# Kernel tuning notes

Measured on AMD Instinct MI355X. Metric: run time of the kernel, lower is better.

The kernel has to match this reference:

```python
import jax, jax.numpy as jnp
import numpy as np

B, L, D, MAXL = 4, 2048, 1024, 4096

def setup_inputs() -> dict:
    key = jax.random.key(0)
    ks = jax.random.split(key, 7)
    x = jax.random.normal(ks[0], (B, L, D), dtype=jnp.float32)
    mask = jnp.ones((B, 1, L), dtype=jnp.int32)
    # kv_proj: Linear(D,D) -> ReLU -> Linear(D, 2D)
    s1 = 1.0 / np.sqrt(D)
    W1 = jax.random.uniform(ks[1], (D, D), minval=-s1, maxval=s1, dtype=jnp.float32)
    b1 = jax.random.uniform(ks[2], (D,), minval=-s1, maxval=s1, dtype=jnp.float32)
    W2 = jax.random.uniform(ks[3], (D, 2 * D), minval=-s1, maxval=s1, dtype=jnp.float32)
    b2 = jax.random.uniform(ks[4], (2 * D,), minval=-s1, maxval=s1, dtype=jnp.float32)
    D_to_L = jax.random.normal(ks[5], (D, MAXL), dtype=jnp.float32) * 0.01
    return {"x": x, "mask": mask, "W1": W1, "b1": b1, "W2": W2, "b2": b2, "D_to_L": D_to_L}

def reference(x, mask, W1, b1, W2, b2, D_to_L):
    Lcur = x.shape[1]
    h = jax.nn.relu(x @ W1 + b1)          # [B,L,D]
    kv = h @ W2 + b2                       # [B,L,2D]
    k, value = jnp.split(kv, 2, axis=-1)   # [B,L,D] each
    scores = jnp.einsum('bld,dk->blk', k, D_to_L[:, :Lcur])  # [B,L,L]
    scores = jnp.where(mask == 0, -jnp.inf, scores)
    attention = jax.nn.softmax(scores, axis=-1)
    output = attention @ value             # [B,L,D]
    return output, attention
```

## Files before the change

kernel.cpp:

```cpp
#include <hip/hip_runtime.h>
#include <cstdint>
#include <cstddef>

__device__ __forceinline__ float bf2f(uint16_t u) {
    union { uint32_t i; float f; } w; w.i = ((uint32_t)u) << 16; return w.f;
}
__device__ __forceinline__ uint16_t f2bf(float f) {
    union { float f; uint32_t i; } w; w.f = f;
    uint32_t x = w.i;
    uint32_t r = (x + 0x7FFFu + ((x >> 16) & 1u)) >> 16;
    return (uint16_t)r;
}

typedef __bf16 bf16x8 __attribute__((ext_vector_type(8)));
typedef float  f32x4  __attribute__((ext_vector_type(4)));

__device__ __forceinline__ void load_lds16(const void* gptr, void* lptr) {
    __builtin_amdgcn_global_load_lds(
        (__attribute__((address_space(1))) void*)gptr,
        (__attribute__((address_space(3))) void*)lptr,
        16, 0, 0);
}

template<int AFP32, int OUTFP32, int RELU>
__global__ __launch_bounds__(256, 3)
void gemm_bt(const void* __restrict__ Av, const uint16_t* __restrict__ BT,
             const float* __restrict__ bias, void* __restrict__ Cv,
             int K, int lda, int ldb, int ldc,
             long long sA, long long sB, long long sC)
{
    __shared__ uint16_t As[128 * 32];
    __shared__ uint16_t Bs[128 * 32];

    const int nx = (int)gridDim.x, ny = (int)gridDim.y, nz = (int)gridDim.z;
    const int g   = (int)blockIdx.x + nx * ((int)blockIdx.y + ny * (int)blockIdx.z);
    const int xcd = g & 7;
    const int ii  = g >> 3;
    const int xz  = 8 / nz;
    const int bz  = xcd / xz;
    const int sub = xcd % xz;
    const int ypc = ny / xz;
    const int by  = sub * ypc + ii % ypc;
    const int bx  = ii / ypc;

    const int t    = threadIdx.x;
    const int lane = t & 63;
    const int w    = t >> 6;
    const int quad = lane >> 4;
    const int l15  = lane & 15;
    const int wr   = w >> 1;
    const int wc   = w & 1;
    const int gm0  = by * 128;
    const int gn0  = bx * 128;

    BT += (long long)bz * sB;

    f32x4 acc[4][4] = {};

    const int ch_r = lane >> 2;
    const int ch_c = (lane & 3) * 8;

    for (int k0 = 0; k0 < K; k0 += 32) {
        __syncthreads();

        {
            int row = w * 16 + ch_r;
            load_lds16(BT + (size_t)(gn0 + row) * ldb + k0 + ch_c, (void*)(Bs + w * 512));
            load_lds16(BT + (size_t)(gn0 + row + 64) * ldb + k0 + ch_c, (void*)(Bs + (w + 4) * 512));
        }
        if (AFP32) {
            const float* A = (const float*)Av + (long long)bz * sA;
            const int row = t >> 1, half = t & 1;
            const float* ap = A + (size_t)(gm0 + row) * lda + k0 + half * 16;
            float4 f0 = ((const float4*)ap)[0];
            float4 f1 = ((const float4*)ap)[1];
            float4 f2 = ((const float4*)ap)[2];
            float4 f3 = ((const float4*)ap)[3];
            union { __bf16 h[16]; uint4 q[2]; } u;
            u.h[0]  = (__bf16)f0.x; u.h[1]  = (__bf16)f0.y;
            u.h[2]  = (__bf16)f0.z; u.h[3]  = (__bf16)f0.w;
            u.h[4]  = (__bf16)f1.x; u.h[5]  = (__bf16)f1.y;
            u.h[6]  = (__bf16)f1.z; u.h[7]  = (__bf16)f1.w;
            u.h[8]  = (__bf16)f2.x; u.h[9]  = (__bf16)f2.y;
            u.h[10] = (__bf16)f2.z; u.h[11] = (__bf16)f2.w;
            u.h[12] = (__bf16)f3.x; u.h[13] = (__bf16)f3.y;
            u.h[14] = (__bf16)f3.z; u.h[15] = (__bf16)f3.w;
            uint4* d = (uint4*)(As + row * 32 + half * 16);
            d[0] = u.q[0];
            d[1] = u.q[1];
        } else {
            const uint16_t* A = (const uint16_t*)Av + (long long)bz * sA;
            int row = w * 16 + ch_r;
            load_lds16(A + (size_t)(gm0 + row) * lda + k0 + ch_c, (void*)(As + w * 512));
            load_lds16(A + (size_t)(gm0 + row + 64) * lda + k0 + ch_c, (void*)(As + (w + 4) * 512));
        }
        __syncthreads();

        bf16x8 af[4], bfr[4];
#pragma unroll
        for (int i = 0; i < 4; i++) {
            af[i]  = *(const bf16x8*)(As + (wr * 64 + i * 16 + l15) * 32 + quad * 8);
            bfr[i] = *(const bf16x8*)(Bs + (wc * 64 + i * 16 + l15) * 32 + quad * 8);
        }
#pragma unroll
        for (int mi = 0; mi < 4; mi++)
#pragma unroll
            for (int ni = 0; ni < 4; ni++)
                acc[mi][ni] = __builtin_amdgcn_mfma_f32_16x16x32_bf16(af[mi], bfr[ni], acc[mi][ni], 0, 0, 0);
    }

#pragma unroll
    for (int ni = 0; ni < 4; ni++) {
        const int gcol = gn0 + wc * 64 + ni * 16 + l15;
        const float bv = bias ? bias[gcol] : 0.0f;
#pragma unroll
        for (int mi = 0; mi < 4; mi++) {
#pragma unroll
            for (int r = 0; r < 4; r++) {
                const int grow = gm0 + wr * 64 + mi * 16 + quad * 4 + r;
                float v = acc[mi][ni][r] + bv;
                if (RELU) v = fmaxf(v, 0.0f);
                if (OUTFP32) {
                    float* C = (float*)Cv + (long long)bz * sC;
                    C[(size_t)grow * ldc + gcol] = v;
                } else {
                    uint16_t* C = (uint16_t*)Cv + (long long)bz * sC;
                    C[(size_t)grow * ldc + gcol] = f2bf(v);
                }
            }
        }
    }
}

__global__ __launch_bounds__(256)
void transpose_f32_to_bf16(const float* __restrict__ src, uint16_t* __restrict__ dst,
                           int src_ld, int dst_ld)
{
    __shared__ uint16_t tile[64 * 65];
    const int k0 = blockIdx.y * 64, n0 = blockIdx.x * 64;
    const int t = threadIdx.x;
#pragma unroll
    for (int i = 0; i < 16; i++) {
        int idx = i * 256 + t;
        int r = idx >> 6, c = idx & 63;
        tile[c * 65 + r] = f2bf(src[(size_t)(k0 + r) * src_ld + n0 + c]);
    }
    __syncthreads();
#pragma unroll
    for (int i = 0; i < 16; i++) {
        int idx = i * 256 + t;
        int n = idx >> 6, k = idx & 63;
        dst[(size_t)(n0 + n) * dst_ld + k0 + k] = tile[n * 65 + k];
    }
}

__global__ __launch_bounds__(256)
void transpose_bf16(const uint16_t* __restrict__ src, uint16_t* __restrict__ dst,
                    int src_ld, int dst_ld, long long sS, long long sD)
{
    __shared__ uint16_t tile[64 * 65];
    src += (long long)blockIdx.z * sS;
    dst += (long long)blockIdx.z * sD;
    const int k0 = blockIdx.y * 64, n0 = blockIdx.x * 64;
    const int t = threadIdx.x;
#pragma unroll
    for (int i = 0; i < 16; i++) {
        int idx = i * 256 + t;
        int r = idx >> 6, c = idx & 63;
        tile[c * 65 + r] = src[(size_t)(k0 + r) * src_ld + n0 + c];
    }
    __syncthreads();
#pragma unroll
    for (int i = 0; i < 16; i++) {
        int idx = i * 256 + t;
        int n = idx >> 6, k = idx & 63;
        dst[(size_t)(n0 + n) * dst_ld + k0 + k] = tile[n * 65 + k];
    }
}

__global__ __launch_bounds__(256)
void softmax_rows_f32(float* __restrict__ S, uint16_t* __restrict__ Sbf,
                      const int* __restrict__ mask, int L)
{
    const int row = blockIdx.x;
    const int b = row >> 11;
    float* rp = S + (size_t)row * L;
    uint16_t* bp = Sbf + (size_t)row * L;
    const int* mrow = mask + (size_t)b * L;
    const int t = threadIdx.x;
    const int c0 = t * 8;

    float v[8];
    *(float4*)(v + 0) = *(const float4*)(rp + c0);
    *(float4*)(v + 4) = *(const float4*)(rp + c0 + 4);
    bool mk[8];
    float lmax = -1e30f;
#pragma unroll
    for (int j = 0; j < 8; j++) {
        mk[j] = (mrow[c0 + j] != 0);
        if (mk[j]) lmax = fmaxf(lmax, v[j]);
    }
#pragma unroll
    for (int off = 32; off > 0; off >>= 1)
        lmax = fmaxf(lmax, __shfl_xor(lmax, off, 64));

    __shared__ float redm[4];
    __shared__ float reds[4];
    const int w = t >> 6, lane = t & 63;
    if (lane == 0) redm[w] = lmax;
    __syncthreads();
    lmax = fmaxf(fmaxf(redm[0], redm[1]), fmaxf(redm[2], redm[3]));

    float e[8];
    float lsum = 0.f;
#pragma unroll
    for (int j = 0; j < 8; j++) {
        e[j] = mk[j] ? __expf(v[j] - lmax) : 0.0f;
        lsum += e[j];
    }
#pragma unroll
    for (int off = 32; off > 0; off >>= 1)
        lsum += __shfl_xor(lsum, off, 64);
    if (lane == 0) reds[w] = lsum;
    __syncthreads();
    lsum = reds[0] + reds[1] + reds[2] + reds[3];

    const float inv = 1.0f / lsum;
    uint16_t ub[8];
#pragma unroll
    for (int j = 0; j < 8; j++) {
        v[j] = e[j] * inv;
        ub[j] = f2bf(v[j]);
    }
    *(float4*)(rp + c0)     = *(const float4*)(v + 0);
    *(float4*)(rp + c0 + 4) = *(const float4*)(v + 4);
    *(uint4*)(bp + c0)      = *(const uint4*)ub;
}

extern "C" void kernel_launch(void* const* d_in, const int* in_sizes, int n_in,
                              void* d_out, int out_size, void* d_ws, size_t ws_size,
                              hipStream_t stream)
{
    const float* x    = (const float*)d_in[0];
    const int*   mask = (const int*)d_in[1];
    const float* W1   = (const float*)d_in[2];
    const float* b1   = (const float*)d_in[3];
    const float* W2   = (const float*)d_in[4];
    const float* b2   = (const float*)d_in[5];
    const float* D2L  = (const float*)d_in[6];

    const int Lr = 2048, D = 1024, M = 4 * Lr;
    float* outp = (float*)d_out;
    float* attn = outp + (size_t)M * D;

    uint16_t* W1T  = (uint16_t*)d_ws;
    uint16_t* W2T  = W1T + 1024 * 1024;
    uint16_t* D2LT = W2T + 2048 * 1024;
    uint16_t* hbuf = D2LT + 2048 * 1024;
    uint16_t* kv   = hbuf + (size_t)M * D;
    uint16_t* vT   = hbuf;
    uint16_t* abf  = kv;

    dim3 blk(256);

    transpose_f32_to_bf16<<<dim3(16, 16), blk, 0, stream>>>(W1,  W1T,  1024, 1024);
    transpose_f32_to_bf16<<<dim3(32, 16), blk, 0, stream>>>(W2,  W2T,  2048, 1024);
    transpose_f32_to_bf16<<<dim3(32, 16), blk, 0, stream>>>(D2L, D2LT, 4096, 1024);

    gemm_bt<1, 0, 1><<<dim3(8, 64, 1), blk, 0, stream>>>(x, W1T, b1, hbuf,
        1024, 1024, 1024, 1024, 0, 0, 0);

    gemm_bt<0, 0, 0><<<dim3(16, 64, 1), blk, 0, stream>>>(hbuf, W2T, b2, kv,
        1024, 1024, 1024, 2048, 0, 0, 0);

    transpose_bf16<<<dim3(16, 32, 4), blk, 0, stream>>>(kv + 1024, vT,
        2048, 2048, (long long)2048 * 2048, (long long)1024 * 2048);

    gemm_bt<0, 1, 0><<<dim3(16, 64, 1), blk, 0, stream>>>(kv, D2LT, nullptr, attn,
        1024, 2048, 1024, 2048, 0, 0, 0);

    softmax_rows_f32<<<dim3(8192), blk, 0, stream>>>(attn, abf, mask, Lr);

    gemm_bt<0, 1, 0><<<dim3(8, 16, 4), blk, 0, stream>>>(abf, vT, nullptr, outp,
        2048, 2048, 2048, 1024,
        (long long)2048 * 2048, (long long)1024 * 2048, (long long)2048 * 1024);
}
```

Measured before the change: 356.4 us.

## Add 256x256 double-buffered GEMM kernel for kv and score projections

```diff
diff --git a/kernel.cpp b/kernel.cpp
--- a/kernel.cpp
+++ b/kernel.cpp
@@ -62,7 +62,6 @@
 
     for (int k0 = 0; k0 < K; k0 += 32) {
         __syncthreads();
-
         {
             int row = w * 16 + ch_r;
             load_lds16(BT + (size_t)(gn0 + row) * ldb + k0 + ch_c, (void*)(Bs + w * 512));
@@ -132,6 +131,122 @@
     }
 }
 
+template<int OUTFP32, int RELU>
+__global__ __launch_bounds__(512, 2)
+void gemm256_bt(const uint16_t* __restrict__ A, const uint16_t* __restrict__ BT,
+                const float* __restrict__ bias, void* __restrict__ Cv,
+                int K, int lda, int ldb, int ldc)
+{
+    extern __shared__ uint16_t lds[];
+
+    const int g   = (int)blockIdx.x + 8 * (int)blockIdx.y;
+    const int xcd = g & 7, ii = g >> 3;
+    const int by  = xcd * 4 + (ii & 3);
+    const int bx  = ii >> 2;
+    const int gm0 = by * 256, gn0 = bx * 256;
+
+    const int t    = threadIdx.x;
+    const int w    = t >> 6, lane = t & 63;
+    const int l15  = lane & 15, quad = lane >> 4;
+    const int wr   = w >> 2, wc = w & 3;
+
+    const int cpr  = quad ^ ((l15 >> 1) & 3);
+    const int arow = wr * 128 + l15;
+    const int brow = wc * 64 + l15;
+
+    const int r0 = t >> 2;
+    const int qg = (t & 3) ^ ((t >> 3) & 3);
+    const uint16_t* aS0 = A  + (size_t)(gm0 + r0) * lda + qg * 8;
+    const uint16_t* aS1 = aS0 + (size_t)128 * lda;
+    const uint16_t* bS0 = BT + (size_t)(gn0 + r0) * ldb + qg * 8;
+    const uint16_t* bS1 = bS0 + (size_t)128 * ldb;
+    const int ldst0 = (w * 64) * 8;
+    const int ldst1 = (512 + w * 64) * 8;
+
+#define SUBA(nb, kh) (lds + ((nb) * 2 + (kh)) * 8192)
+#define SUBB(nb, kh) (lds + 32768 + ((nb) * 2 + (kh)) * 8192)
+#define STAGE_A(nb, kh, k0s) do {                                              \
+        load_lds16(aS0 + (k0s) + (kh) * 32, (void*)(SUBA(nb, kh) + ldst0));    \
+        load_lds16(aS1 + (k0s) + (kh) * 32, (void*)(SUBA(nb, kh) + ldst1));    \
+    } while (0)
+#define STAGE_B(nb, kh, k0s) do {                                              \
+        load_lds16(bS0 + (k0s) + (kh) * 32, (void*)(SUBB(nb, kh) + ldst0));    \
+        load_lds16(bS1 + (k0s) + (kh) * 32, (void*)(SUBB(nb, kh) + ldst1));    \
+    } while (0)
+#define VMWAIT4 asm volatile("s_waitcnt vmcnt(4)" ::: "memory")
+#define NOWAIT  ((void)0)
+
+    f32x4 acc[8][4] = {};
+    bf16x8 bF[4];
+
+    STAGE_A(0, 0, 0); STAGE_B(0, 0, 0); STAGE_A(0, 1, 0); STAGE_B(0, 1, 0);
+    VMWAIT4;
+    __builtin_amdgcn_s_barrier();
+
+    const int NT = K >> 6;
+    for (int kt = 0; kt < NT; ++kt) {
+        const int buf = kt & 1, nb = buf ^ 1;
+        const int nk0 = (kt + 1 < NT) ? ((kt + 1) << 6) : 0;
+
+#define PHASE(kh, mh, STAGE_STMT, VM_STMT)                                          \
+        {                                                                           \
+            const uint16_t* As_ = SUBA(buf, kh);                                    \
+            const uint16_t* Bs_ = SUBB(buf, kh);                                    \
+            bf16x8 aF[4];                                                           \
+            _Pragma("unroll")                                                       \
+            for (int i = 0; i < 4; i++)                                             \
+                aF[i] = *(const bf16x8*)(As_ + (arow + (mh) * 64 + i * 16) * 32 + cpr * 8); \
+            if ((mh) == 0) {                                                        \
+                _Pragma("unroll")                                                   \
+                for (int ni = 0; ni < 4; ni++)                                      \
+                    bF[ni] = *(const bf16x8*)(Bs_ + (brow + ni * 16) * 32 + cpr * 8); \
+            }                                                                       \
+            STAGE_STMT;                                                             \
+            __builtin_amdgcn_s_barrier();                                           \
+            __builtin_amdgcn_s_setprio(1);                                          \
+            _Pragma("unroll")                                                       \
+            for (int i = 0; i < 4; i++)                                             \
+                _Pragma("unroll")                                                   \
+                for (int ni = 0; ni < 4; ni++)                                      \
+                    acc[(mh) * 4 + i][ni] = __builtin_amdgcn_mfma_f32_16x16x32_bf16( \
+                        aF[i], bF[ni], acc[(mh) * 4 + i][ni], 0, 0, 0);             \
+            __builtin_amdgcn_s_setprio(0);                                          \
+            VM_STMT;                                                                \
+            __builtin_amdgcn_s_barrier();                                           \
+        }
+
+        PHASE(0, 0, STAGE_A(nb, 0, nk0), NOWAIT)
+        PHASE(0, 1, STAGE_B(nb, 0, nk0), VMWAIT4)
+        PHASE(1, 0, STAGE_A(nb, 1, nk0), NOWAIT)
+        PHASE(1, 1, STAGE_B(nb, 1, nk0), VMWAIT4)
+#undef PHASE
+    }
+    asm volatile("s_waitcnt vmcnt(0)" ::: "memory");
+
+#pragma unroll
+    for (int ni = 0; ni < 4; ni++) {
+        const int gcol = gn0 + wc * 64 + ni * 16 + l15;
+        const float bv = bias ? bias[gcol] : 0.0f;
+#pragma unroll
+        for (int mi = 0; mi < 8; mi++) {
+#pragma unroll
+            for (int r = 0; r < 4; r++) {
+                const int grow = gm0 + wr * 128 + mi * 16 + quad * 4 + r;
+                float v = acc[mi][ni][r] + bv;
+                if (RELU) v = fmaxf(v, 0.0f);
+                if (OUTFP32) ((float*)Cv)[(size_t)grow * ldc + gcol] = v;
+                else         ((uint16_t*)Cv)[(size_t)grow * ldc + gcol] = f2bf(v);
+            }
+        }
+    }
+#undef SUBA
+#undef SUBB
+#undef STAGE_A
+#undef STAGE_B
+#undef VMWAIT4
+#undef NOWAIT
+}
+
 __global__ __launch_bounds__(256)
 void transpose_f32_to_bf16(const float* __restrict__ src, uint16_t* __restrict__ dst,
                            int src_ld, int dst_ld)
@@ -263,6 +378,11 @@
 
     dim3 blk(256);
 
+    hipFuncSetAttribute(reinterpret_cast<const void*>(&gemm256_bt<0, 0>),
+                        hipFuncAttributeMaxDynamicSharedMemorySize, 131072);
+    hipFuncSetAttribute(reinterpret_cast<const void*>(&gemm256_bt<1, 0>),
+                        hipFuncAttributeMaxDynamicSharedMemorySize, 131072);
+
     transpose_f32_to_bf16<<<dim3(16, 16), blk, 0, stream>>>(W1,  W1T,  1024, 1024);
     transpose_f32_to_bf16<<<dim3(32, 16), blk, 0, stream>>>(W2,  W2T,  2048, 1024);
     transpose_f32_to_bf16<<<dim3(32, 16), blk, 0, stream>>>(D2L, D2LT, 4096, 1024);
@@ -270,14 +390,14 @@
     gemm_bt<1, 0, 1><<<dim3(8, 64, 1), blk, 0, stream>>>(x, W1T, b1, hbuf,
         1024, 1024, 1024, 1024, 0, 0, 0);
 
-    gemm_bt<0, 0, 0><<<dim3(16, 64, 1), blk, 0, stream>>>(hbuf, W2T, b2, kv,
-        1024, 1024, 1024, 2048, 0, 0, 0);
+    gemm256_bt<0, 0><<<dim3(8, 32), dim3(512), 131072, stream>>>(hbuf, W2T, b2, kv,
+        1024, 1024, 1024, 2048);
 
     transpose_bf16<<<dim3(16, 32, 4), blk, 0, stream>>>(kv + 1024, vT,
         2048, 2048, (long long)2048 * 2048, (long long)1024 * 2048);
 
-    gemm_bt<0, 1, 0><<<dim3(16, 64, 1), blk, 0, stream>>>(kv, D2LT, nullptr, attn,
-        1024, 2048, 1024, 2048, 0, 0, 0);
+    gemm256_bt<1, 0><<<dim3(8, 32), dim3(512), 131072, stream>>>(kv, D2LT, nullptr, attn,
+        1024, 2048, 1024, 2048);
 
     softmax_rows_f32<<<dim3(8192), blk, 0, stream>>>(attn, abf, mask, Lr);
 
```

New measurement: 350.2 us. About the same (-1.8%).

## Replace GEMMs with 256-row double-buffered swizzled-LDS pipelined kernel

Applied to the files above, without the earlier changes.

```diff
diff --git a/kernel.cpp b/kernel.cpp
--- a/kernel.cpp
+++ b/kernel.cpp
@@ -2,9 +2,6 @@
 #include <cstdint>
 #include <cstddef>
 
-__device__ __forceinline__ float bf2f(uint16_t u) {
-    union { uint32_t i; float f; } w; w.i = ((uint32_t)u) << 16; return w.f;
-}
 __device__ __forceinline__ uint16_t f2bf(float f) {
     union { float f; uint32_t i; } w; w.f = f;
     uint32_t x = w.i;
@@ -22,114 +19,179 @@
         16, 0, 0);
 }
 
-template<int AFP32, int OUTFP32, int RELU>
-__global__ __launch_bounds__(256, 3)
-void gemm_bt(const void* __restrict__ Av, const uint16_t* __restrict__ BT,
+template<int BN, int OUTFP32, int RELU>
+__global__ __launch_bounds__(512, 2)
+void gemm256(const uint16_t* __restrict__ A, const uint16_t* __restrict__ BT,
              const float* __restrict__ bias, void* __restrict__ Cv,
              int K, int lda, int ldb, int ldc,
-             long long sA, long long sB, long long sC)
-{
-    __shared__ uint16_t As[128 * 32];
-    __shared__ uint16_t Bs[128 * 32];
-
-    const int nx = (int)gridDim.x, ny = (int)gridDim.y, nz = (int)gridDim.z;
-    const int g   = (int)blockIdx.x + nx * ((int)blockIdx.y + ny * (int)blockIdx.z);
-    const int xcd = g & 7;
-    const int ii  = g >> 3;
-    const int xz  = 8 / nz;
-    const int bz  = xcd / xz;
-    const int sub = xcd % xz;
-    const int ypc = ny / xz;
-    const int by  = sub * ypc + ii % ypc;
-    const int bx  = ii / ypc;
+             long long sB, int byShift)
+{
+    extern __shared__ uint16_t lds[];
+    constexpr int SB  = (BN == 256) ? 2 : 1;
+    constexpr int WN  = BN / 64;
+    constexpr int MI  = 2 * WN;
+    constexpr int SBE = BN * 32;
+
+    const int g   = (int)blockIdx.x + (int)gridDim.x * (int)blockIdx.y;
+    const int xcd = g & 7, ii = g >> 3;
+    const int by  = xcd * 4 + (ii & 3);
+    const int bx  = ii >> 2;
+    const int gm0 = by * 256, gn0 = bx * BN;
+    const int bz  = by >> byShift;
+    BT += (long long)bz * sB;
 
     const int t    = threadIdx.x;
-    const int lane = t & 63;
-    const int w    = t >> 6;
-    const int quad = lane >> 4;
-    const int l15  = lane & 15;
-    const int wr   = w >> 1;
-    const int wc   = w & 1;
-    const int gm0  = by * 128;
-    const int gn0  = bx * 128;
-
-    BT += (long long)bz * sB;
-
-    f32x4 acc[4][4] = {};
-
-    const int ch_r = lane >> 2;
-    const int ch_c = (lane & 3) * 8;
-
-    for (int k0 = 0; k0 < K; k0 += 32) {
-        __syncthreads();
-
-        {
-            int row = w * 16 + ch_r;
-            load_lds16(BT + (size_t)(gn0 + row) * ldb + k0 + ch_c, (void*)(Bs + w * 512));
-            load_lds16(BT + (size_t)(gn0 + row + 64) * ldb + k0 + ch_c, (void*)(Bs + (w + 4) * 512));
+    const int w    = t >> 6, lane = t & 63;
+    const int l15  = lane & 15, quad = lane >> 4;
+    const int wr   = w / WN, wc = w % WN;
+
+    const int cpr  = quad ^ ((l15 >> 1) & 3);
+    const int arow = wr * (32 * WN) + l15;
+    const int brow = wc * 64 + l15;
+
+    const int r0 = t >> 2;
+    const int qg = (t & 3) ^ ((t >> 3) & 3);
+    const uint16_t* aS0 = A  + (size_t)(gm0 + r0) * lda + qg * 8;
+    const uint16_t* aS1 = aS0 + (size_t)128 * lda;
+    const uint16_t* bS0 = BT + (size_t)(gn0 + r0) * ldb + qg * 8;
+    const uint16_t* bS1 = bS0 + (size_t)128 * ldb;
+    const int ldw = w * 512;
+
+#define SUBA(nb, kh) (lds + ((nb) * 2 + (kh)) * 8192)
+#define SUBB(nb, kh) (lds + 32768 + ((nb) * 2 + (kh)) * SBE)
+#define STAGE_A(nb, kh, k0s) do {                                               \
+        load_lds16(aS0 + (k0s) + (kh) * 32, (void*)(SUBA(nb, kh) + ldw));       \
+        load_lds16(aS1 + (k0s) + (kh) * 32, (void*)(SUBA(nb, kh) + 4096 + ldw));\
+    } while (0)
+#define STAGE_B(nb, kh, k0s) do {                                               \
+        load_lds16(bS0 + (k0s) + (kh) * 32, (void*)(SUBB(nb, kh) + ldw));       \
+        if constexpr (BN == 256)                                                \
+            load_lds16(bS1 + (k0s) + (kh) * 32,                                 \
+                       (void*)(SUBB(nb, kh) + 4096 + ldw));                     \
+    } while (0)
+#define VMW do {                                                                \
+        if constexpr (SB == 2) asm volatile("s_waitcnt vmcnt(4)" ::: "memory"); \
+        else                   asm volatile("s_waitcnt vmcnt(3)" ::: "memory"); \
+    } while (0)
+#define LGKM0 asm volatile("s_waitcnt lgkmcnt(0)" ::: "memory")
+#define NOWAIT ((void)0)
+
+    f32x4 acc[MI][4] = {};
+    bf16x8 bF[4];
+
+    STAGE_A(0, 0, 0); STAGE_B(0, 0, 0); STAGE_A(0, 1, 0); STAGE_B(0, 1, 0);
+    VMW;
+    __builtin_amdgcn_s_barrier();
+
+    const int NT = K >> 6;
+    for (int kt = 0; kt < NT; ++kt) {
+        const int buf = kt & 1, nb = buf ^ 1;
+        const int nk0 = (kt + 1 < NT) ? ((kt + 1) << 6) : 0;
+
+        if constexpr (BN == 256) {
+#define PHASE256(kh, mh, STAGE_STMT, VM_STMT)                                       \
+            {                                                                       \
+                const uint16_t* As_ = SUBA(buf, kh);                                \
+                const uint16_t* Bs_ = SUBB(buf, kh);                                \
+                bf16x8 aF[4];                                                       \
+                _Pragma("unroll")                                                   \
+                for (int i = 0; i < 4; i++)                                         \
+                    aF[i] = *(const bf16x8*)(As_ + (arow + (mh) * 64 + i * 16) * 32 + cpr * 8); \
+                if ((mh) == 0) {                                                    \
+                    _Pragma("unroll")                                               \
+                    for (int ni = 0; ni < 4; ni++)                                  \
+                        bF[ni] = *(const bf16x8*)(Bs_ + (brow + ni * 16) * 32 + cpr * 8); \
+                }                                                                   \
+                STAGE_STMT;                                                         \
+                __builtin_amdgcn_s_barrier();                                       \
+                LGKM0;                                                              \
+                __builtin_amdgcn_s_setprio(1);                                      \
+                _Pragma("unroll")                                                   \
+                for (int i = 0; i < 4; i++)                                         \
+                    _Pragma("unroll")                                               \
+                    for (int ni = 0; ni < 4; ni++)                                  \
+                        acc[(mh) * 4 + i][ni] = __builtin_amdgcn_mfma_f32_16x16x32_bf16( \
+                            aF[i], bF[ni], acc[(mh) * 4 + i][ni], 0, 0, 0);         \
+                __builtin_amdgcn_s_setprio(0);                                      \
+                VM_STMT;                                                            \
+                __builtin_amdgcn_s_barrier();                                       \
+            }
+            PHASE256(0, 0, STAGE_A(nb, 0, nk0), NOWAIT)
+            PHASE256(0, 1, STAGE_B(nb, 0, nk0), VMW)
+            PHASE256(1, 0, STAGE_A(nb, 1, nk0), NOWAIT)
+            PHASE256(1, 1, STAGE_B(nb, 1, nk0), VMW)
+#undef PHASE256
+        } else {
+#define PHASE128(kh)                                                                \
+            {                                                                       \
+                const uint16_t* As_ = SUBA(buf, kh);                                \
+                const uint16_t* Bs_ = SUBB(buf, kh);                                \
+                bf16x8 aF[4], bG[4];                                                \
+                _Pragma("unroll")                                                   \
+                for (int i = 0; i < 4; i++)                                         \
+                    aF[i] = *(const bf16x8*)(As_ + (arow + i * 16) * 32 + cpr * 8); \
+                _Pragma("unroll")                                                   \
+                for (int ni = 0; ni < 4; ni++)                                      \
+                    bG[ni] = *(const bf16x8*)(Bs_ + (brow + ni * 16) * 32 + cpr * 8); \
+                STAGE_A(nb, kh, nk0);                                               \
+                STAGE_B(nb, kh, nk0);                                               \
+                __builtin_amdgcn_s_barrier();                                       \
+                LGKM0;                                                              \
+                __builtin_amdgcn_s_setprio(1);                                      \
+                _Pragma("unroll")                                                   \
+                for (int i = 0; i < 4; i++)                                         \
+                    _Pragma("unroll")                                               \
+                    for (int ni = 0; ni < 4; ni++)                                  \
+                        acc[i][ni] = __builtin_amdgcn_mfma_f32_16x16x32_bf16(       \
+                            aF[i], bG[ni], acc[i][ni], 0, 0, 0);                    \
+                __builtin_amdgcn_s_setprio(0);                                      \
+                VMW;                                                                \
+                __builtin_amdgcn_s_barrier();                                       \
+            }
+            PHASE128(0)
+            PHASE128(1)
+#undef PHASE128
         }
-        if (AFP32) {
-            const float* A = (const float*)Av + (long long)bz * sA;
-            const int row = t >> 1, half = t & 1;
-            const float* ap = A + (size_t)(gm0 + row) * lda + k0 + half * 16;
-            float4 f0 = ((const float4*)ap)[0];
-            float4 f1 = ((const float4*)ap)[1];
-            float4 f2 = ((const float4*)ap)[2];
-            float4 f3 = ((const float4*)ap)[3];
-            union { __bf16 h[16]; uint4 q[2]; } u;
-            u.h[0]  = (__bf16)f0.x; u.h[1]  = (__bf16)f0.y;
-            u.h[2]  = (__bf16)f0.z; u.h[3]  = (__bf16)f0.w;
-            u.h[4]  = (__bf16)f1.x; u.h[5]  = (__bf16)f1.y;
-            u.h[6]  = (__bf16)f1.z; u.h[7]  = (__bf16)f1.w;
-            u.h[8]  = (__bf16)f2.x; u.h[9]  = (__bf16)f2.y;
-            u.h[10] = (__bf16)f2.z; u.h[11] = (__bf16)f2.w;
-            u.h[12] = (__bf16)f3.x; u.h[13] = (__bf16)f3.y;
-            u.h[14] = (__bf16)f3.z; u.h[15] = (__bf16)f3.w;
-            uint4* d = (uint4*)(As + row * 32 + half * 16);
-            d[0] = u.q[0];
-            d[1] = u.q[1];
-        } else {
-            const uint16_t* A = (const uint16_t*)Av + (long long)bz * sA;
-            int row = w * 16 + ch_r;
-            load_lds16(A + (size_t)(gm0 + row) * lda + k0 + ch_c, (void*)(As + w * 512));
-            load_lds16(A + (size_t)(gm0 + row + 64) * lda + k0 + ch_c, (void*)(As + (w + 4) * 512));
-        }
-        __syncthreads();
-
-        bf16x8 af[4], bfr[4];
-#pragma unroll
-        for (int i = 0; i < 4; i++) {
-            af[i]  = *(const bf16x8*)(As + (wr * 64 + i * 16 + l15) * 32 + quad * 8);
-            bfr[i] = *(const bf16x8*)(Bs + (wc * 64 + i * 16 + l15) * 32 + quad * 8);
-        }
-#pragma unroll
-        for (int mi = 0; mi < 4; mi++)
-#pragma unroll
-            for (int ni = 0; ni < 4; ni++)
-                acc[mi][ni] = __builtin_amdgcn_mfma_f32_16x16x32_bf16(af[mi], bfr[ni], acc[mi][ni], 0, 0, 0);
-    }
+    }
+    asm volatile("s_waitcnt vmcnt(0)" ::: "memory");
 
 #pragma unroll
     for (int ni = 0; ni < 4; ni++) {
         const int gcol = gn0 + wc * 64 + ni * 16 + l15;
         const float bv = bias ? bias[gcol] : 0.0f;
 #pragma unroll
-        for (int mi = 0; mi < 4; mi++) {
+        for (int mi = 0; mi < MI; mi++) {
 #pragma unroll
             for (int r = 0; r < 4; r++) {
-                const int grow = gm0 + wr * 64 + mi * 16 + quad * 4 + r;
+                const int grow = gm0 + wr * (32 * WN) + mi * 16 + quad * 4 + r;
                 float v = acc[mi][ni][r] + bv;
                 if (RELU) v = fmaxf(v, 0.0f);
-                if (OUTFP32) {
-                    float* C = (float*)Cv + (long long)bz * sC;
-                    C[(size_t)grow * ldc + gcol] = v;
-                } else {
-                    uint16_t* C = (uint16_t*)Cv + (long long)bz * sC;
-                    C[(size_t)grow * ldc + gcol] = f2bf(v);
-                }
+                if (OUTFP32) ((float*)Cv)[(size_t)grow * ldc + gcol] = v;
+                else         ((uint16_t*)Cv)[(size_t)grow * ldc + gcol] = f2bf(v);
             }
         }
     }
+#undef SUBA
+#undef SUBB
+#undef STAGE_A
+#undef STAGE_B
+#undef VMW
+#undef LGKM0
+#undef NOWAIT
+}
+
+__global__ __launch_bounds__(256)
+void cast_f32_bf16(const float* __restrict__ src, uint16_t* __restrict__ dst)
+{
+    const size_t i = ((size_t)blockIdx.x * 256 + threadIdx.x) * 8;
+    float4 a = *(const float4*)(src + i);
+    float4 b = *(const float4*)(src + i + 4);
+    union { __bf16 h[8]; uint4 q; } u;
+    u.h[0] = (__bf16)a.x; u.h[1] = (__bf16)a.y;
+    u.h[2] = (__bf16)a.z; u.h[3] = (__bf16)a.w;
+    u.h[4] = (__bf16)b.x; u.h[5] = (__bf16)b.y;
+    u.h[6] = (__bf16)b.z; u.h[7] = (__bf16)b.w;
+    *(uint4*)(dst + i) = u.q;
 }
 
 __global__ __launch_bounds__(256)
@@ -258,30 +320,42 @@
     uint16_t* D2LT = W2T + 2048 * 1024;
     uint16_t* hbuf = D2LT + 2048 * 1024;
     uint16_t* kv   = hbuf + (size_t)M * D;
+    uint16_t* xbf  = kv + (size_t)M * 2048;
     uint16_t* vT   = hbuf;
     uint16_t* abf  = kv;
 
     dim3 blk(256);
+    const dim3 g256(8, 32), b512(512);
+
+    hipFuncSetAttribute(reinterpret_cast<const void*>(&gemm256<256, 0, 0>),
+                        hipFuncAttributeMaxDynamicSharedMemorySize, 131072);
+    hipFuncSetAttribute(reinterpret_cast<const void*>(&gemm256<256, 1, 0>),
+                        hipFuncAttributeMaxDynamicSharedMemorySize, 131072);
+    hipFuncSetAttribute(reinterpret_cast<const void*>(&gemm256<128, 0, 1>),
+                        hipFuncAttributeMaxDynamicSharedMemorySize, 98304);
+    hipFuncSetAttribute(reinterpret_cast<const void*>(&gemm256<128, 1, 0>),
+                        hipFuncAttributeMaxDynamicSharedMemorySize, 98304);
+
+    cast_f32_bf16<<<dim3(4096), blk, 0, stream>>>(x, xbf);
 
     transpose_f32_to_bf16<<<dim3(16, 16), blk, 0, stream>>>(W1,  W1T,  1024, 1024);
     transpose_f32_to_bf16<<<dim3(32, 16), blk, 0, stream>>>(W2,  W2T,  2048, 1024);
     transpose_f32_to_bf16<<<dim3(32, 16), blk, 0, stream>>>(D2L, D2LT, 4096, 1024);
 
-    gemm_bt<1, 0, 1><<<dim3(8, 64, 1), blk, 0, stream>>>(x, W1T, b1, hbuf,
-        1024, 1024, 1024, 1024, 0, 0, 0);
-
-    gemm_bt<0, 0, 0><<<dim3(16, 64, 1), blk, 0, stream>>>(hbuf, W2T, b2, kv,
-        1024, 1024, 1024, 2048, 0, 0, 0);
+    gemm256<128, 0, 1><<<g256, b512, 98304, stream>>>(xbf, W1T, b1, hbuf,
+        1024, 1024, 1024, 1024, 0, 30);
+
+    gemm256<256, 0, 0><<<g256, b512, 131072, stream>>>(hbuf, W2T, b2, kv,
+        1024, 1024, 1024, 2048, 0, 30);
 
     transpose_bf16<<<dim3(16, 32, 4), blk, 0, stream>>>(kv + 1024, vT,
         2048, 2048, (long long)2048 * 2048, (long long)1024 * 2048);
 
-    gemm_bt<0, 1, 0><<<dim3(16, 64, 1), blk, 0, stream>>>(kv, D2LT, nullptr, attn,
-        1024, 2048, 1024, 2048, 0, 0, 0);
+    gemm256<256, 1, 0><<<g256, b512, 131072, stream>>>(kv, D2LT, nullptr, attn,
+        1024, 2048, 1024, 2048, 0, 30);
 
     softmax_rows_f32<<<dim3(8192), blk, 0, stream>>>(attn, abf, mask, Lr);
 
-    gemm_bt<0, 1, 0><<<dim3(8, 16, 4), blk, 0, stream>>>(abf, vT, nullptr, outp,
-        2048, 2048, 2048, 1024,
-        (long long)2048 * 2048, (long long)1024 * 2048, (long long)2048 * 1024);
-}
+    gemm256<128, 1, 0><<<g256, b512, 98304, stream>>>(abf, vT, nullptr, outp,
+        2048, 2048, 2048, 1024, (long long)1024 * 2048, 3);
+}
```

Result: faster. 328.4 us (-7.9%).
